# Kernel optimization log

Hardware: AMD Instinct MI355X
Metric: run time of the kernel (lower is better)

## Reference

```python
import jax, jax.numpy as jnp
import numpy as np

B, N, D, H = 256, 196, 384, 1536  # batch, patches, dim, mlp hidden


def fake_quant(w, bits):
    """Symmetric per-tensor uniform fake quantization with straight-through estimator."""
    qmax = 2.0 ** (bits - 1) - 1.0
    scale = jnp.maximum(jnp.max(jnp.abs(w)) / qmax, 1e-8)
    q = jnp.clip(jnp.round(w / scale), -qmax, qmax) * scale
    return w + jax.lax.stop_gradient(q - w)


def setup_inputs() -> dict:
    key = jax.random.key(0)
    ks = jax.random.split(key, 8)
    return {
        "x": jax.random.normal(ks[0], (B, N, D), jnp.float32),
        "alpha1": jnp.ones((D,), jnp.float32),
        "beta1": jnp.zeros((D,), jnp.float32),
        "W_attn": jax.random.normal(ks[1], (N, N), jnp.float32) * (1.0 / np.sqrt(N)),
        "b_attn": jnp.zeros((N,), jnp.float32),
        "gamma1": jax.random.uniform(ks[2], (D,), jnp.float32) * 0.1,
        "alpha2": jnp.ones((D,), jnp.float32),
        "beta2": jnp.zeros((D,), jnp.float32),
        "W1": jax.random.normal(ks[3], (H, D), jnp.float32) * (1.0 / np.sqrt(D)),
        "b1": jnp.zeros((H,), jnp.float32),
        "W2": jax.random.normal(ks[4], (D, H), jnp.float32) * (1.0 / np.sqrt(H)),
        "b2": jnp.zeros((D,), jnp.float32),
        "gamma2": jax.random.uniform(ks[5], (D,), jnp.float32) * 0.1,
        "bits": 8,
    }


def reference(x, alpha1, beta1, W_attn, b_attn, gamma1,
              alpha2, beta2, W1, b1, W2, b2, gamma2, bits):
    # --- token-mixing branch ---
    org = x
    h = alpha1 * x + beta1                                   # Aff norm1, [B,N,D]
    # transpose(1,2) -> [B,D,N]; Linear(N,N); transpose back == einsum over patch dim
    Wq = fake_quant(W_attn, bits)
    h = jnp.einsum('bnd,mn->bmd', h, Wq) + b_attn[:, None]   # [B,N,D], bias per patch
    x = gamma1 * h + org                                     # layerscale + residual
    # --- channel-mixing branch ---
    org = x
    h = alpha2 * x + beta2                                   # Aff norm2
    h = jax.nn.gelu(h @ fake_quant(W1, bits).T + b1)         # [B,N,H]
    h = h @ fake_quant(W2, bits).T + b2                      # [B,N,D]
    return gamma2 * h + org
```

## Files before the change

### kernel.cpp

```cpp
#include <hip/hip_runtime.h>
#include <hip/hip_bf16.h>
#include <stdint.h>

#define Bb 256
#define Nn 196
#define Dd 384
#define Hh 1536
#define NPAD 224
#define MPAD 256
#define TTOT (Bb*Nn)
#define XLD 232
#define TK 128
#define HS 128

typedef __attribute__((ext_vector_type(8))) __bf16 bf16x8;
typedef __attribute__((ext_vector_type(4))) float f32x4;

#define GLD16(gp, lp) __builtin_amdgcn_global_load_lds( \
    (const __attribute__((address_space(1))) void*)(gp), \
    (__attribute__((address_space(3))) void*)(lp), 16, 0, 0)

#define MFMA16(a, b, c) __builtin_amdgcn_mfma_f32_16x16x32_bf16((a), (b), (c), 0, 0, 0)

__device__ __forceinline__ ushort f2bf(float f){
  union { float f; unsigned u; } v; v.f = f;
  unsigned r = v.u + 0x7FFFu + ((v.u >> 16) & 1u);
  return (ushort)(r >> 16);
}

__global__ void absmax3_k(const float* __restrict__ wa, const float* __restrict__ w1,
                          const float* __restrict__ w2, unsigned* __restrict__ out){
  int which = blockIdx.y;
  const float* w = which == 0 ? wa : (which == 1 ? w1 : w2);
  int n = which == 0 ? Nn*Nn : Hh*Dd;
  float m = 0.f;
  for (int i = blockIdx.x*blockDim.x + threadIdx.x; i < n; i += gridDim.x*blockDim.x)
    m = fmaxf(m, fabsf(w[i]));
  #pragma unroll
  for (int o = 32; o >= 1; o >>= 1) m = fmaxf(m, __shfl_xor(m, o));
  __shared__ float sm[4];
  if ((threadIdx.x & 63) == 0) sm[threadIdx.x >> 6] = m;
  __syncthreads();
  if (threadIdx.x == 0){
    float mm = fmaxf(fmaxf(sm[0], sm[1]), fmaxf(sm[2], sm[3]));
    atomicMax(out + which, __float_as_uint(mm));
  }
}

__global__ void quant_all_k(const float* __restrict__ Wa, const float* __restrict__ W1,
                            const float* __restrict__ W2, const unsigned* __restrict__ amax,
                            const int* __restrict__ bitsp,
                            ushort* __restrict__ Wq, ushort* __restrict__ W1q,
                            ushort* __restrict__ W2q){
  const int which = blockIdx.y;
  const int idx = blockIdx.x*256 + threadIdx.x;
  const float qmax = (float)((1 << (bitsp[0]-1)) - 1);
  const float s = fmaxf(__uint_as_float(amax[which]) / qmax, 1e-8f);
  if (which == 0){
    if (idx >= MPAD*NPAD) return;
    int m = idx / NPAD, n = idx - m*NPAD;
    float v = 0.f;
    if (m < Nn && n < Nn){
      float q = fminf(fmaxf(rintf(Wa[m*Nn + n] / s), -qmax), qmax);
      v = q * s;
    }
    Wq[idx] = f2bf(v);
  } else {
    const float* W = (which == 1) ? W1 : W2;
    ushort* Wo = (which == 1) ? W1q : W2q;
    float q = fminf(fmaxf(rintf(W[idx] / s), -qmax), qmax);
    Wo[idx] = f2bf(q * s);
  }
}

__global__ __launch_bounds__(256, 2) void gemm1_k(const ushort* __restrict__ Wq,
    const float* __restrict__ x,
    const float* __restrict__ alpha1, const float* __restrict__ beta1,
    const float* __restrict__ b_attn, const float* __restrict__ gamma1,
    const float* __restrict__ alpha2, const float* __restrict__ beta2,
    float* __restrict__ x1, ushort* __restrict__ hn2){
  __shared__ ushort Xs[128*XLD];
  const int tid = threadIdx.x;
  const int b = blockIdx.y, dt = blockIdx.x, d0 = dt*128;

  {
    const int dme = tid & 127;
    const int ng  = tid >> 7;
    const float a1 = alpha1[d0 + dme], be1 = beta1[d0 + dme];
    const float* xcol = x + (long)b*Nn*Dd + d0 + dme;
    #pragma unroll
    for (int p = 0; p < 14; p++){
      const int n0 = (p*2 + ng)*8;
      ushort o[8];
      #pragma unroll
      for (int t = 0; t < 8; t++){
        const int n = n0 + t;
        float v = 0.f;
        if (n < Nn) v = fmaf(a1, xcol[(long)n*Dd], be1);
        o[t] = f2bf(v);
      }
      *(int4*)&Xs[dme*XLD + n0] = *(int4*)o;
    }
  }
  __syncthreads();

  const int lane = tid & 63;
  const int wr = (tid >> 7) & 1, wc = (tid >> 6) & 1;
  const int arow = lane & 15, koff = (lane >> 4)*8;
  const int g = lane >> 4;
  for (int mt = 0; mt < 2; mt++){
    f32x4 acc[4][4] = {};
    #pragma unroll
    for (int k7 = 0; k7 < 7; k7++){
      bf16x8 ag[4], bg[4];
      #pragma unroll
      for (int i=0;i<4;i++){
        int row = mt*128 + wr*64 + i*16 + arow;
        ag[i] = *(const bf16x8*)&Wq[row*NPAD + k7*32 + koff];
        bg[i] = *(const bf16x8*)&Xs[(wc*64 + i*16 + arow)*XLD + k7*32 + koff];
      }
      #pragma unroll
      for (int i=0;i<4;i++)
        #pragma unroll
        for (int j=0;j<4;j++)
          acc[i][j] = MFMA16(bg[i], ag[j], acc[i][j]);
    }
    #pragma unroll
    for (int i=0;i<4;i++){
      const int d = d0 + wc*64 + i*16 + g*4;
      const float4 g1 = *(const float4*)&gamma1[d];
      const float4 a2 = *(const float4*)&alpha2[d];
      const float4 b2v = *(const float4*)&beta2[d];
      #pragma unroll
      for (int j=0;j<4;j++){
        const int m = mt*128 + wr*64 + j*16 + arow;
        if (m < Nn){
          const long base = ((long)b*Nn + m)*Dd + d;
          const float4 xv = *(const float4*)&x[base];
          const float ba = b_attn[m];
          float4 o;
          o.x = fmaf(g1.x, acc[i][j][0] + ba, xv.x);
          o.y = fmaf(g1.y, acc[i][j][1] + ba, xv.y);
          o.z = fmaf(g1.z, acc[i][j][2] + ba, xv.z);
          o.w = fmaf(g1.w, acc[i][j][3] + ba, xv.w);
          *(float4*)&x1[base] = o;
          ushort h4[4];
          h4[0] = f2bf(fmaf(a2.x, o.x, b2v.x));
          h4[1] = f2bf(fmaf(a2.y, o.y, b2v.y));
          h4[2] = f2bf(fmaf(a2.z, o.z, b2v.z));
          h4[3] = f2bf(fmaf(a2.w, o.w, b2v.w));
          *(int2*)&hn2[base] = *(int2*)h4;
        }
      }
    }
  }
}


__device__ __forceinline__ void stage_A(const ushort* __restrict__ hn2t,
                                        const ushort* __restrict__ W1q, int hs, int ka,
                                        ushort* slot){
  const int tid = threadIdx.x;
  const int r  = tid >> 3;
  const int us = ((tid & 7) ^ (r & 7)) * 8;
  const int k0 = ka*64;
  const ushort* w1 = W1q + (long)hs*HS*Dd + k0;
  GLD16(hn2t + (long)r*Dd + k0 + us,        slot + tid*8);
  GLD16(hn2t + (long)(r+64)*Dd + k0 + us,   slot + 4096 + tid*8);
  GLD16(w1 + (long)r*Dd + us,               slot + 8192 + tid*8);
  GLD16(w1 + (long)(r+64)*Dd + us,          slot + 12288 + tid*8);
}

__device__ __forceinline__ void stage_B(const ushort* __restrict__ W2q, int hs, int kb,
                                        ushort* slot){
  const int tid = threadIdx.x;
  const int r  = tid >> 2;
  const int us = ((tid & 3) ^ ((r >> 1) & 3)) * 8;
  const ushort* w2 = W2q + hs*HS + kb*32;
  GLD16(w2 + (long)r*Hh + us,          slot + tid*8);
  GLD16(w2 + (long)(r+128)*Hh + us,    slot + 4096 + tid*8);
  GLD16(w2 + (long)(r+256)*Hh + us,    slot + 8192 + tid*8);
}

__global__ __launch_bounds__(512, 2) void mlp_k(const ushort* __restrict__ hn2,
    const ushort* __restrict__ W1q, const ushort* __restrict__ W2q,
    const float* __restrict__ b1, const float* __restrict__ b2,
    const float* __restrict__ gamma2, float* __restrict__ out){
  __shared__ ushort SH[49152];
  ushort* const buf0 = SH;
  ushort* const buf1 = SH + 16384;
  ushort* const Ps   = SH + 32768;

  const int tid  = threadIdx.x;
  const int lane = tid & 63;
  const int wv   = tid >> 6;
  const int wt   = wv >> 2;
  const int wh   = wv & 3;
  const int arow = lane & 15;
  const int a7   = arow & 7;
  const int g    = lane >> 4;
  const long t0  = (long)blockIdx.x * TK;
  const ushort* hn2t = hn2 + t0*Dd;

  stage_A(hn2t, W1q, 0, 0, buf0);
  __syncthreads();

  f32x4 oacc[4][6] = {};
  int cur = 0;

  for (int hs = 0; hs < 12; ++hs){
    f32x4 pacc[4][2] = {};
    #pragma unroll
    for (int ka = 0; ka < 6; ++ka){
      ushort* nslot = cur ? buf0 : buf1;
      if (ka < 5) stage_A(hn2t, W1q, hs, ka+1, nslot);
      else        stage_B(W2q, hs, 0, nslot);
      const ushort* Asl = cur ? buf1 : buf0;
      const ushort* W1l = Asl + 8192;
      bf16x8 ag[4][2], bg[2][2];
      #pragma unroll
      for (int ks=0; ks<2; ks++){
        const int cu8 = ((ks*4 + g) ^ a7) * 8;
        #pragma unroll
        for (int i=0;i<4;i++)
          ag[i][ks] = *(const bf16x8*)&Asl[(wt*64 + i*16 + arow)*64 + cu8];
        #pragma unroll
        for (int j=0;j<2;j++)
          bg[j][ks] = *(const bf16x8*)&W1l[(wh*32 + j*16 + arow)*64 + cu8];
      }
      __builtin_amdgcn_s_setprio(1);
      #pragma unroll
      for (int ks=0;ks<2;ks++)
        #pragma unroll
        for (int i=0;i<4;i++)
          #pragma unroll
          for (int j=0;j<2;j++)
            pacc[i][j] = MFMA16(ag[i][ks], bg[j][ks], pacc[i][j]);
      __builtin_amdgcn_s_setprio(0);
      __syncthreads();
      cur ^= 1;
    }
    #pragma unroll
    for (int j=0;j<2;j++){
      int hcol = wh*32 + j*16 + arow;
      float b1v = b1[hs*HS + hcol];
      #pragma unroll
      for (int i=0;i<4;i++){
        #pragma unroll
        for (int r=0;r<4;r++){
          int row = wt*64 + i*16 + g*4 + r;
          float v = pacc[i][j][r] + b1v;
          float u = 0.7978845608028654f * v * fmaf(0.044715f, v*v, 1.f);
          float gl = v / (1.f + __expf(-2.f*u));
          Ps[row*HS + (hcol ^ ((row & 7) << 3))] = f2bf(gl);
        }
      }
    }
    __syncthreads();
    #pragma unroll
    for (int kb = 0; kb < 4; ++kb){
      ushort* nslot = cur ? buf0 : buf1;
      if (kb < 3) stage_B(W2q, hs, kb+1, nslot);
      else        stage_A(hn2t, W1q, (hs+1) % 12, 0, nslot);
      const ushort* W2l = cur ? buf1 : buf0;
      bf16x8 pa[4], bgb[6];
      #pragma unroll
      for (int i=0;i<4;i++){
        int row = wt*64 + i*16 + arow;
        pa[i] = *(const bf16x8*)&Ps[row*HS + ((kb*32 + g*8) ^ (a7 << 3))];
      }
      const int u8 = (g ^ ((arow >> 1) & 3)) * 8;
      #pragma unroll
      for (int j=0;j<6;j++)
        bgb[j] = *(const bf16x8*)&W2l[(wh*96 + j*16 + arow)*32 + u8];
      __builtin_amdgcn_s_setprio(1);
      #pragma unroll
      for (int i=0;i<4;i++)
        #pragma unroll
        for (int j=0;j<6;j++)
          oacc[i][j] = MFMA16(pa[i], bgb[j], oacc[i][j]);
      __builtin_amdgcn_s_setprio(0);
      __syncthreads();
      cur ^= 1;
    }
  }

  #pragma unroll
  for (int i=0;i<4;i++){
    #pragma unroll
    for (int j=0;j<6;j++){
      int d = wh*96 + j*16 + arow;
      float g2 = gamma2[d], b2v = b2[d];
      #pragma unroll
      for (int r=0;r<4;r++){
        long t = t0 + wt*64 + i*16 + g*4 + r;
        long idx = t*Dd + d;
        out[idx] = fmaf(g2, oacc[i][j][r] + b2v, out[idx]);
      }
    }
  }
}

extern "C" void kernel_launch(void* const* d_in, const int* in_sizes, int n_in,
                              void* d_out, int out_size, void* d_ws, size_t ws_size,
                              hipStream_t stream){
  const float* x      = (const float*)d_in[0];
  const float* alpha1 = (const float*)d_in[1];
  const float* beta1  = (const float*)d_in[2];
  const float* W_attn = (const float*)d_in[3];
  const float* b_attn = (const float*)d_in[4];
  const float* gamma1 = (const float*)d_in[5];
  const float* alpha2 = (const float*)d_in[6];
  const float* beta2  = (const float*)d_in[7];
  const float* W1     = (const float*)d_in[8];
  const float* b1     = (const float*)d_in[9];
  const float* W2     = (const float*)d_in[10];
  const float* b2     = (const float*)d_in[11];
  const float* gamma2 = (const float*)d_in[12];
  const int*   bits   = (const int*)d_in[13];

  char* ws = (char*)d_ws;
  unsigned* amax = (unsigned*)ws;
  ushort* Wq   = (ushort*)(ws + 256);
  ushort* W1q  = (ushort*)(ws + 114944);
  ushort* W2q  = (ushort*)(ws + 1294592);
  ushort* hn2  = (ushort*)(ws + 2474240);
  float*  x1   = (float*)d_out;

  hipMemsetAsync(amax, 0, 256, stream);
  absmax3_k<<<dim3(128, 3), 256, 0, stream>>>(W_attn, W1, W2, amax);
  quant_all_k<<<dim3((Hh*Dd)/256, 3), 256, 0, stream>>>(W_attn, W1, W2, amax, bits,
                                                        Wq, W1q, W2q);
  gemm1_k<<<dim3(3, Bb), 256, 0, stream>>>(Wq, x, alpha1, beta1, b_attn, gamma1,
                                           alpha2, beta2, x1, hn2);
  mlp_k<<<TTOT/TK, 512, 0, stream>>>(hn2, W1q, W2q, b1, b2, gamma2, (float*)d_out);
}
```

Measured before the change: 322.2 us.

## Store residual intermediate in bf16 and vectorize MLP epilogue via swapped MFMA operands

New measurement: 361.9 us. +12.3%, slower.

```diff
diff --git a/kernel.cpp b/kernel.cpp
--- a/kernel.cpp
+++ b/kernel.cpp
@@ -27,15 +27,20 @@
   unsigned r = v.u + 0x7FFFu + ((v.u >> 16) & 1u);
   return (ushort)(r >> 16);
 }
+__device__ __forceinline__ float bf2f(ushort u){
+  union { unsigned u; float f; } v; v.u = ((unsigned)u) << 16; return v.f;
+}
 
 __global__ void absmax3_k(const float* __restrict__ wa, const float* __restrict__ w1,
                           const float* __restrict__ w2, unsigned* __restrict__ out){
   int which = blockIdx.y;
-  const float* w = which == 0 ? wa : (which == 1 ? w1 : w2);
-  int n = which == 0 ? Nn*Nn : Hh*Dd;
+  const float4* w = (const float4*)(which == 0 ? wa : (which == 1 ? w1 : w2));
+  int n4 = (which == 0 ? Nn*Nn : Hh*Dd) >> 2;
   float m = 0.f;
-  for (int i = blockIdx.x*blockDim.x + threadIdx.x; i < n; i += gridDim.x*blockDim.x)
-    m = fmaxf(m, fabsf(w[i]));
+  for (int i = blockIdx.x*blockDim.x + threadIdx.x; i < n4; i += gridDim.x*blockDim.x){
+    float4 v = w[i];
+    m = fmaxf(m, fmaxf(fmaxf(fabsf(v.x), fabsf(v.y)), fmaxf(fabsf(v.z), fabsf(v.w))));
+  }
   #pragma unroll
   for (int o = 32; o >= 1; o >>= 1) m = fmaxf(m, __shfl_xor(m, o));
   __shared__ float sm[4];
@@ -78,7 +83,7 @@
     const float* __restrict__ alpha1, const float* __restrict__ beta1,
     const float* __restrict__ b_attn, const float* __restrict__ gamma1,
     const float* __restrict__ alpha2, const float* __restrict__ beta2,
-    float* __restrict__ x1, ushort* __restrict__ hn2){
+    ushort* __restrict__ x1b, ushort* __restrict__ hn2){
   __shared__ ushort Xs[128*XLD];
   const int tid = threadIdx.x;
   const int b = blockIdx.y, dt = blockIdx.x, d0 = dt*128;
@@ -143,7 +148,9 @@
           o.y = fmaf(g1.y, acc[i][j][1] + ba, xv.y);
           o.z = fmaf(g1.z, acc[i][j][2] + ba, xv.z);
           o.w = fmaf(g1.w, acc[i][j][3] + ba, xv.w);
-          *(float4*)&x1[base] = o;
+          ushort xo[4];
+          xo[0] = f2bf(o.x); xo[1] = f2bf(o.y); xo[2] = f2bf(o.z); xo[3] = f2bf(o.w);
+          *(int2*)&x1b[base] = *(int2*)xo;
           ushort h4[4];
           h4[0] = f2bf(fmaf(a2.x, o.x, b2v.x));
           h4[1] = f2bf(fmaf(a2.y, o.y, b2v.y));
@@ -185,7 +192,8 @@
 __global__ __launch_bounds__(512, 2) void mlp_k(const ushort* __restrict__ hn2,
     const ushort* __restrict__ W1q, const ushort* __restrict__ W2q,
     const float* __restrict__ b1, const float* __restrict__ b2,
-    const float* __restrict__ gamma2, float* __restrict__ out){
+    const float* __restrict__ gamma2, const ushort* __restrict__ x1b,
+    float* __restrict__ out){
   __shared__ ushort SH[49152];
   ushort* const buf0 = SH;
   ushort* const buf1 = SH + 16384;
@@ -205,7 +213,7 @@
   stage_A(hn2t, W1q, 0, 0, buf0);
   __syncthreads();
 
-  f32x4 oacc[4][6] = {};
+  f32x4 oacc[6][4] = {};
   int cur = 0;
 
   for (int hs = 0; hs < 12; ++hs){
@@ -275,10 +283,10 @@
         bgb[j] = *(const bf16x8*)&W2l[(wh*96 + j*16 + arow)*32 + u8];
       __builtin_amdgcn_s_setprio(1);
       #pragma unroll
-      for (int i=0;i<4;i++)
-        #pragma unroll
-        for (int j=0;j<6;j++)
-          oacc[i][j] = MFMA16(pa[i], bgb[j], oacc[i][j]);
+      for (int j=0;j<6;j++)
+        #pragma unroll
+        for (int i=0;i<4;i++)
+          oacc[j][i] = MFMA16(bgb[j], pa[i], oacc[j][i]);
       __builtin_amdgcn_s_setprio(0);
       __syncthreads();
       cur ^= 1;
@@ -286,17 +294,21 @@
   }
 
   #pragma unroll
-  for (int i=0;i<4;i++){
-    #pragma unroll
-    for (int j=0;j<6;j++){
-      int d = wh*96 + j*16 + arow;
-      float g2 = gamma2[d], b2v = b2[d];
-      #pragma unroll
-      for (int r=0;r<4;r++){
-        long t = t0 + wt*64 + i*16 + g*4 + r;
-        long idx = t*Dd + d;
-        out[idx] = fmaf(g2, oacc[i][j][r] + b2v, out[idx]);
-      }
+  for (int i=0;i<6;i++){
+    const int d = wh*96 + i*16 + g*4;
+    const float4 g2 = *(const float4*)&gamma2[d];
+    const float4 bv = *(const float4*)&b2[d];
+    #pragma unroll
+    for (int j=0;j<4;j++){
+      const long tok = t0 + wt*64 + j*16 + arow;
+      const long base = tok*Dd + d;
+      const int2 xi = *(const int2*)&x1b[base];
+      float4 o;
+      o.x = fmaf(g2.x, oacc[i][j][0] + bv.x, bf2f((ushort)(xi.x & 0xffff)));
+      o.y = fmaf(g2.y, oacc[i][j][1] + bv.y, bf2f((ushort)(((unsigned)xi.x) >> 16)));
+      o.z = fmaf(g2.z, oacc[i][j][2] + bv.z, bf2f((ushort)(xi.y & 0xffff)));
+      o.w = fmaf(g2.w, oacc[i][j][3] + bv.w, bf2f((ushort)(((unsigned)xi.y) >> 16)));
+      *(float4*)&out[base] = o;
     }
   }
 }
@@ -325,13 +337,13 @@
   ushort* W1q  = (ushort*)(ws + 114944);
   ushort* W2q  = (ushort*)(ws + 1294592);
   ushort* hn2  = (ushort*)(ws + 2474240);
-  float*  x1   = (float*)d_out;
+  ushort* x1b  = (ushort*)(ws + 41009408);
 
   hipMemsetAsync(amax, 0, 256, stream);
   absmax3_k<<<dim3(128, 3), 256, 0, stream>>>(W_attn, W1, W2, amax);
   quant_all_k<<<dim3((Hh*Dd)/256, 3), 256, 0, stream>>>(W_attn, W1, W2, amax, bits,
                                                         Wq, W1q, W2q);
   gemm1_k<<<dim3(3, Bb), 256, 0, stream>>>(Wq, x, alpha1, beta1, b_attn, gamma1,
-                                           alpha2, beta2, x1, hn2);
-  mlp_k<<<TTOT/TK, 512, 0, stream>>>(hn2, W1q, W2q, b1, b2, gamma2, (float*)d_out);
-}
+                                           alpha2, beta2, x1b, hn2);
+  mlp_k<<<TTOT/TK, 512, 0, stream>>>(hn2, W1q, W2q, b1, b2, gamma2, x1b, (float*)d_out);
+}
```
